# Performance work log

Hardware: AMD Instinct MI355X
Metric: run time of the kernel (lower is better)

## Reference

```python
import jax, jax.numpy as jnp
import numpy as np

N_NODES = 100000
N_EDGES = 3200000


def setup_inputs() -> dict:
    key = jax.random.key(0)
    ks = jax.random.split(key, 12)
    x = jax.random.normal(ks[0], (N_NODES, 34), dtype=jnp.float32)
    edge_index = jax.random.randint(ks[1], (2, N_EDGES), 0, N_NODES, dtype=jnp.int64)
    def lin(k, fin, fout):
        s = 1.0 / np.sqrt(fin)
        kw, kb = jax.random.split(k)
        W = jax.random.uniform(kw, (fin, fout), jnp.float32, -s, s)
        b = jax.random.uniform(kb, (fout,), jnp.float32, -s, s)
        return W, b
    W1, b1 = lin(ks[2], 34, 64)
    W2, b2 = lin(ks[3], 64, 32)
    W3, b3 = lin(ks[4], 32, 16)
    W4, b4 = lin(ks[5], 16, 8)
    Wc, bc = lin(ks[6], 8, 2)
    return {"x": x, "edge_index": edge_index,
            "W1": W1, "b1": b1, "W2": W2, "b2": b2,
            "W3": W3, "b3": b3, "W4": W4, "b4": b4,
            "Wc": Wc, "bc": bc}


def _gcn_norm(edge_index, n_nodes):
    # PyG GCNConv: add self-loops, symmetric normalization D^-1/2 (A+I) D^-1/2
    loop = jnp.arange(n_nodes, dtype=edge_index.dtype)
    src = jnp.concatenate([edge_index[0], loop])  # [E+N]
    dst = jnp.concatenate([edge_index[1], loop])
    deg = jax.ops.segment_sum(jnp.ones_like(dst, dtype=jnp.float32), dst,
                              num_segments=n_nodes)
    dinv = jnp.where(deg > 0, jax.lax.rsqrt(deg), 0.0)
    norm = dinv[src] * dinv[dst]  # [E+N]
    return src, dst, norm


def _gcn_conv(h, W, b, src, dst, norm, n_nodes):
    h = h @ W                                    # [N, Fout] small GEMM
    msg = h[src] * norm[:, None]                 # gather + scale
    out = jax.ops.segment_sum(msg, dst, num_segments=n_nodes)  # scatter-add
    return out + b


def reference(x, edge_index, W1, b1, W2, b2, W3, b3, W4, b4, Wc, bc):
    n = x.shape[0]
    src, dst, norm = _gcn_norm(edge_index, n)
    h = jnp.tanh(_gcn_conv(x, W1, b1, src, dst, norm, n))
    h = jnp.tanh(_gcn_conv(h, W2, b2, src, dst, norm, n))
    h = jnp.tanh(_gcn_conv(h, W3, b3, src, dst, norm, n))
    h = jnp.tanh(_gcn_conv(h, W4, b4, src, dst, norm, n))
    out = h @ Wc + bc
    return (out, h)
```

## Files before the change

kernel.cpp:

```cpp
#include <hip/hip_runtime.h>
#include <math.h>

#define N_NODES 100000
#define BSHIFT 8
#define BNODES 256
#define NB ((N_NODES + BNODES - 1) / BNODES)
#define CHUNK 8192


__device__ __forceinline__ unsigned short f2bf(float x) {
    unsigned u = __float_as_uint(x);
    u += 0x7FFFu + ((u >> 16) & 1u);
    return (unsigned short)(u >> 16);
}
__device__ __forceinline__ unsigned pack2(float a, float b) {
    return (unsigned)f2bf(a) | ((unsigned)f2bf(b) << 16);
}
__device__ __forceinline__ float bflo(unsigned u) { return __uint_as_float(u << 16); }
__device__ __forceinline__ float bfhi(unsigned u) { return __uint_as_float(u & 0xFFFF0000u); }
__device__ __forceinline__ int nt_ld(const int* p) { return __builtin_nontemporal_load(p); }


__global__ __launch_bounds__(256) void bucket_count(const int* __restrict__ dst,
                                                    int* __restrict__ bucketCount, int E) {
    __shared__ int hist[NB];
    for (int i = threadIdx.x; i < NB; i += 256) hist[i] = 0;
    __syncthreads();
    int i = blockIdx.x * blockDim.x + threadIdx.x;
    int stride = gridDim.x * blockDim.x;
    for (int e = i; e < E; e += stride)
        atomicAdd(&hist[nt_ld(dst + e) >> BSHIFT], 1);
    __syncthreads();
    for (int i2 = threadIdx.x; i2 < NB; i2 += 256) {
        int c = hist[i2];
        if (c) atomicAdd(&bucketCount[i2], c);
    }
}


__global__ __launch_bounds__(512) void bucket_scan(const int* __restrict__ bucketCount,
                                                   int* __restrict__ bucketOff,
                                                   int* __restrict__ bucketCursor, int E) {
    __shared__ int sh[512];
    int t = threadIdx.x;
    int v = (t < NB) ? bucketCount[t] : 0;
    sh[t] = v;
    __syncthreads();
    for (int d = 1; d < 512; d <<= 1) {
        int u = (t >= d) ? sh[t - d] : 0;
        __syncthreads();
        sh[t] += u;
        __syncthreads();
    }
    if (t < NB) { bucketOff[t] = sh[t] - v; bucketCursor[t] = sh[t] - v; }
    if (t == 0) bucketOff[NB] = E;
}


__global__ __launch_bounds__(256) void bucket_fill(const int* __restrict__ src,
                                                   const int* __restrict__ dst,
                                                   int* __restrict__ bucketCursor,
                                                   unsigned int* __restrict__ binned, int E) {
    __shared__ int hist[NB];
    __shared__ int base[NB];
    __shared__ int lcur[NB];
    __shared__ unsigned int recs[CHUNK];
    __shared__ unsigned short bkt[CHUNK];
    int t = threadIdx.x;
    for (int i = t; i < NB; i += 256) { hist[i] = 0; lcur[i] = 0; }
    __syncthreads();
    int cbase = blockIdx.x * CHUNK;
#pragma unroll
    for (int j = 0; j < CHUNK / 256; ++j) {
        int slot = t + j * 256;
        int e = cbase + slot;
        if (e < E) {
            int s = nt_ld(src + e);
            int d = nt_ld(dst + e);
            recs[slot] = (unsigned)s | ((unsigned)(d & (BNODES - 1)) << 17);
            int b = d >> BSHIFT;
            bkt[slot] = (unsigned short)b;
            atomicAdd(&hist[b], 1);
        } else {
            bkt[slot] = 0xFFFF;
        }
    }
    __syncthreads();
    for (int i = t; i < NB; i += 256) {
        int c = hist[i];
        base[i] = c ? atomicAdd(&bucketCursor[i], c) : 0;
    }
    __syncthreads();
#pragma unroll
    for (int j = 0; j < CHUNK / 256; ++j) {
        int slot = t + j * 256;
        unsigned short b = bkt[slot];
        if (b != 0xFFFF) {
            int pos = base[b] + atomicAdd(&lcur[b], 1);
            binned[pos] = recs[slot];
        }
    }
}


__global__ __launch_bounds__(256) void node_off_sort(const unsigned int* __restrict__ binned,
                                                     const int* __restrict__ bucketOff,
                                                     int* __restrict__ off,
                                                     float* __restrict__ dinv,
                                                     int* __restrict__ srcs, int n, int E) {
    __shared__ int hist[BNODES];
    __shared__ int sh[BNODES];
    __shared__ int lcur[BNODES];
    int t = threadIdx.x;
    int b = blockIdx.x;
    hist[t] = 0;
    __syncthreads();
    int rb = bucketOff[b], re = bucketOff[b + 1];
    for (int e = rb + t; e < re; e += 256)
        atomicAdd(&hist[(binned[e] >> 17) & 255], 1);
    __syncthreads();
    int v = hist[t];
    sh[t] = v;
    __syncthreads();
    for (int d = 1; d < 256; d <<= 1) {
        int u = (t >= d) ? sh[t - d] : 0;
        __syncthreads();
        sh[t] += u;
        __syncthreads();
    }
    int base = rb + sh[t] - v;
    lcur[t] = base;
    int g = b * BNODES + t;
    if (g < n) {
        off[g] = base;
        dinv[g] = rsqrtf((float)v + 1.0f);
    }
    if (b == NB - 1 && t == 0) off[n] = E;
    __syncthreads();
    for (int e = rb + t; e < re; e += 256) {
        unsigned int r = binned[e];
        int pos = atomicAdd(&lcur[(r >> 17) & 255], 1);
        srcs[pos] = (int)(r & 0x1FFFF);
    }
}


__global__ void x_pack(const float* __restrict__ x, const float* __restrict__ dinv,
                       unsigned* __restrict__ xm, unsigned* __restrict__ xt, int n) {
    int i = blockIdx.x * blockDim.x + threadIdx.x;
    if (i >= n) return;
    float dv = dinv[i];
    const float2* xr = (const float2*)(x + (size_t)i * 34);
    unsigned* om = xm + (size_t)i * 16;
#pragma unroll
    for (int j = 0; j < 16; ++j) { float2 v = xr[j]; om[j] = pack2(dv * v.x, dv * v.y); }
    float2 v = xr[16];
    xt[i] = pack2(dv * v.x, dv * v.y);
}


__global__ __launch_bounds__(256) void gather_x_bf16(const int* __restrict__ off,
        const int* __restrict__ srcs, const unsigned* __restrict__ xm,
        const unsigned* __restrict__ xt, const float* __restrict__ dinv,
        float* __restrict__ aggx, int n) {
    int g = blockIdx.x * 16 + (threadIdx.x >> 4);
    int f = threadIdx.x & 15;
    if (g >= n) return;
    int rb = off[g], re = off[g + 1];
    unsigned ug = xm[(size_t)g * 16 + f];
    float a0 = bflo(ug), a1 = bfhi(ug);
    float a2 = 0.f, a3 = 0.f;
    if (f == 0) { unsigned tt = xt[g]; a2 = bflo(tt); a3 = bfhi(tt); }
    int e = rb;
    for (; e + 8 <= re; e += 8) {
        int s0 = nt_ld(srcs + e),     s1 = nt_ld(srcs + e + 1);
        int s2 = nt_ld(srcs + e + 2), s3 = nt_ld(srcs + e + 3);
        int s4 = nt_ld(srcs + e + 4), s5 = nt_ld(srcs + e + 5);
        int s6 = nt_ld(srcs + e + 6), s7 = nt_ld(srcs + e + 7);
        unsigned u0 = xm[(size_t)s0 * 16 + f], u1 = xm[(size_t)s1 * 16 + f];
        unsigned u2 = xm[(size_t)s2 * 16 + f], u3 = xm[(size_t)s3 * 16 + f];
        unsigned u4 = xm[(size_t)s4 * 16 + f], u5 = xm[(size_t)s5 * 16 + f];
        unsigned u6 = xm[(size_t)s6 * 16 + f], u7 = xm[(size_t)s7 * 16 + f];
        a0 += bflo(u0); a1 += bfhi(u0); a0 += bflo(u1); a1 += bfhi(u1);
        a0 += bflo(u2); a1 += bfhi(u2); a0 += bflo(u3); a1 += bfhi(u3);
        a0 += bflo(u4); a1 += bfhi(u4); a0 += bflo(u5); a1 += bfhi(u5);
        a0 += bflo(u6); a1 += bfhi(u6); a0 += bflo(u7); a1 += bfhi(u7);
        if (f == 0) {
            unsigned t0 = xt[s0], t1 = xt[s1], t2 = xt[s2], t3 = xt[s3];
            unsigned t4 = xt[s4], t5 = xt[s5], t6 = xt[s6], t7 = xt[s7];
            a2 += bflo(t0); a3 += bfhi(t0); a2 += bflo(t1); a3 += bfhi(t1);
            a2 += bflo(t2); a3 += bfhi(t2); a2 += bflo(t3); a3 += bfhi(t3);
            a2 += bflo(t4); a3 += bfhi(t4); a2 += bflo(t5); a3 += bfhi(t5);
            a2 += bflo(t6); a3 += bfhi(t6); a2 += bflo(t7); a3 += bfhi(t7);
        }
    }
    for (; e < re; ++e) {
        int s = nt_ld(srcs + e);
        unsigned u = xm[(size_t)s * 16 + f];
        a0 += bflo(u); a1 += bfhi(u);
        if (f == 0) { unsigned tt = xt[s]; a2 += bflo(tt); a3 += bfhi(tt); }
    }
    float dv = dinv[g];
    *(float2*)(aggx + (size_t)g * 34 + 2 * f) = make_float2(dv * a0, dv * a1);
    if (f == 0) *(float2*)(aggx + (size_t)g * 34 + 32) = make_float2(dv * a2, dv * a3);
}


#define G12_BLOCKS 2048

__global__ __launch_bounds__(256) void gemm12(const float* __restrict__ aggx,
        const float* __restrict__ W1, const float* __restrict__ b1,
        const float* __restrict__ W2, const float* __restrict__ dinv,
        unsigned* __restrict__ linh2, int n) {
    __shared__ float sW1t[64 * 34];
    __shared__ float sW2[64 * 32];
    __shared__ float sh1[16][64];
    for (int i = threadIdx.x; i < 34 * 64; i += 256) {
        int k = i >> 6, j = i & 63;
        sW1t[j * 34 + k] = W1[i];
    }
    for (int i = threadIdx.x; i < 64 * 32; i += 256) sW2[i] = W2[i];
    __syncthreads();
    int j  = threadIdx.x & 63;
    int rq = threadIdx.x >> 6;
    int p  = threadIdx.x & 15;
    int r2 = threadIdx.x >> 4;
    float bj = b1[j];
    const float2* w1v = (const float2*)(sW1t + j * 34);
    const float2* w2v = (const float2*)sW2;
    for (int base = blockIdx.x * 16; base < n; base += G12_BLOCKS * 16) {
#pragma unroll
        for (int q = 0; q < 4; ++q) {
            int r = rq * 4 + q;
            int row = base + r;
            float h1v = 0.f;
            if (row < n) {
                const float2* hr = (const float2*)(aggx + (size_t)row * 34);
                float acc = 0.f;
#pragma unroll
                for (int k2 = 0; k2 < 17; ++k2) {
                    float2 wv = w1v[k2];
                    float2 hv = hr[k2];
                    acc = fmaf(hv.x, wv.x, acc);
                    acc = fmaf(hv.y, wv.y, acc);
                }
                h1v = tanhf(acc + bj);
            }
            sh1[r][j] = h1v;
        }
        __syncthreads();
        {
            int row = base + r2;
            if (row < n) {
                const float2* sh1v = (const float2*)&sh1[r2][0];
                float a0 = 0.f, a1 = 0.f;
#pragma unroll
                for (int k2 = 0; k2 < 32; ++k2) {
                    float2 h = sh1v[k2];
                    float2 wa = w2v[(2 * k2) * 16 + p];
                    float2 wb = w2v[(2 * k2 + 1) * 16 + p];
                    a0 = fmaf(h.x, wa.x, a0); a1 = fmaf(h.x, wa.y, a1);
                    a0 = fmaf(h.y, wb.x, a0); a1 = fmaf(h.y, wb.y, a1);
                }
                float dv = dinv[row];
                linh2[(size_t)row * 16 + p] = pack2(dv * a0, dv * a1);
            }
        }
        __syncthreads();
    }
}


__global__ __launch_bounds__(256) void gather2_proj(const int* __restrict__ off,
        const int* __restrict__ srcs, const unsigned* __restrict__ linh2,
        const float* __restrict__ dinv, const float* __restrict__ b2,
        const float* __restrict__ W3, unsigned* __restrict__ linh3, int n) {
    __shared__ float sW3[32 * 16];
    for (int i = threadIdx.x; i < 32 * 16; i += 256) sW3[i] = W3[i];
    __syncthreads();
    int g = blockIdx.x * 16 + (threadIdx.x >> 4);
    int f = threadIdx.x & 15;
    if (g >= n) return;
    int rb = off[g], re = off[g + 1];
    unsigned ug = linh2[(size_t)g * 16 + f];
    float a0 = bflo(ug), a1 = bfhi(ug);
    int e = rb;
    for (; e + 8 <= re; e += 8) {
        int s0 = nt_ld(srcs + e),     s1 = nt_ld(srcs + e + 1);
        int s2 = nt_ld(srcs + e + 2), s3 = nt_ld(srcs + e + 3);
        int s4 = nt_ld(srcs + e + 4), s5 = nt_ld(srcs + e + 5);
        int s6 = nt_ld(srcs + e + 6), s7 = nt_ld(srcs + e + 7);
        unsigned u0 = linh2[(size_t)s0 * 16 + f], u1 = linh2[(size_t)s1 * 16 + f];
        unsigned u2 = linh2[(size_t)s2 * 16 + f], u3 = linh2[(size_t)s3 * 16 + f];
        unsigned u4 = linh2[(size_t)s4 * 16 + f], u5 = linh2[(size_t)s5 * 16 + f];
        unsigned u6 = linh2[(size_t)s6 * 16 + f], u7 = linh2[(size_t)s7 * 16 + f];
        a0 += bflo(u0); a1 += bfhi(u0); a0 += bflo(u1); a1 += bfhi(u1);
        a0 += bflo(u2); a1 += bfhi(u2); a0 += bflo(u3); a1 += bfhi(u3);
        a0 += bflo(u4); a1 += bfhi(u4); a0 += bflo(u5); a1 += bfhi(u5);
        a0 += bflo(u6); a1 += bfhi(u6); a0 += bflo(u7); a1 += bfhi(u7);
    }
    for (; e < re; ++e) {
        int s = nt_ld(srcs + e);
        unsigned u = linh2[(size_t)s * 16 + f];
        a0 += bflo(u); a1 += bfhi(u);
    }
    float dv = dinv[g];
    float h0 = tanhf(fmaf(dv, a0, b2[2 * f]));
    float h1 = tanhf(fmaf(dv, a1, b2[2 * f + 1]));
    float p[16];
#pragma unroll
    for (int o = 0; o < 16; ++o)
        p[o] = h0 * sW3[(2 * f) * 16 + o] + h1 * sW3[(2 * f + 1) * 16 + o];
#pragma unroll
    for (int m = 1; m <= 8; m <<= 1)
#pragma unroll
        for (int o = 0; o < 16; ++o) p[o] += __shfl_xor(p[o], m);
    if (f < 8) linh3[(size_t)g * 8 + f] = pack2(dv * p[2 * f], dv * p[2 * f + 1]);
}


__global__ __launch_bounds__(256) void gather3_proj(const int* __restrict__ off,
        const int* __restrict__ srcs, const unsigned* __restrict__ linh3,
        const float* __restrict__ dinv, const float* __restrict__ b3,
        const float* __restrict__ W4, unsigned* __restrict__ linh4, int n) {
    __shared__ float sW4[16 * 8];
    for (int i = threadIdx.x; i < 16 * 8; i += 256) sW4[i] = W4[i];
    __syncthreads();
    int g = blockIdx.x * 32 + (threadIdx.x >> 3);
    int f = threadIdx.x & 7;
    if (g >= n) return;
    int rb = off[g], re = off[g + 1];
    unsigned ug = linh3[(size_t)g * 8 + f];
    float a0 = bflo(ug), a1 = bfhi(ug);
    int e = rb;
    for (; e + 8 <= re; e += 8) {
        int s0 = nt_ld(srcs + e),     s1 = nt_ld(srcs + e + 1);
        int s2 = nt_ld(srcs + e + 2), s3 = nt_ld(srcs + e + 3);
        int s4 = nt_ld(srcs + e + 4), s5 = nt_ld(srcs + e + 5);
        int s6 = nt_ld(srcs + e + 6), s7 = nt_ld(srcs + e + 7);
        unsigned u0 = linh3[(size_t)s0 * 8 + f], u1 = linh3[(size_t)s1 * 8 + f];
        unsigned u2 = linh3[(size_t)s2 * 8 + f], u3 = linh3[(size_t)s3 * 8 + f];
        unsigned u4 = linh3[(size_t)s4 * 8 + f], u5 = linh3[(size_t)s5 * 8 + f];
        unsigned u6 = linh3[(size_t)s6 * 8 + f], u7 = linh3[(size_t)s7 * 8 + f];
        a0 += bflo(u0); a1 += bfhi(u0); a0 += bflo(u1); a1 += bfhi(u1);
        a0 += bflo(u2); a1 += bfhi(u2); a0 += bflo(u3); a1 += bfhi(u3);
        a0 += bflo(u4); a1 += bfhi(u4); a0 += bflo(u5); a1 += bfhi(u5);
        a0 += bflo(u6); a1 += bfhi(u6); a0 += bflo(u7); a1 += bfhi(u7);
    }
    for (; e < re; ++e) {
        int s = nt_ld(srcs + e);
        unsigned u = linh3[(size_t)s * 8 + f];
        a0 += bflo(u); a1 += bfhi(u);
    }
    float dv = dinv[g];
    float h0 = tanhf(fmaf(dv, a0, b3[2 * f]));
    float h1 = tanhf(fmaf(dv, a1, b3[2 * f + 1]));
    float p[8];
#pragma unroll
    for (int o = 0; o < 8; ++o)
        p[o] = h0 * sW4[(2 * f) * 8 + o] + h1 * sW4[(2 * f + 1) * 8 + o];
#pragma unroll
    for (int m = 1; m <= 4; m <<= 1)
#pragma unroll
        for (int o = 0; o < 8; ++o) p[o] += __shfl_xor(p[o], m);
    if (f < 4) linh4[(size_t)g * 4 + f] = pack2(dv * p[2 * f], dv * p[2 * f + 1]);
}


__global__ __launch_bounds__(256) void gather4_cls(const int* __restrict__ off,
        const int* __restrict__ srcs, const unsigned* __restrict__ linh4,
        const float* __restrict__ dinv, const float* __restrict__ b4,
        float* __restrict__ hout, const float* __restrict__ Wc,
        const float* __restrict__ bc, float* __restrict__ out, int n) {
    int g = blockIdx.x * 64 + (threadIdx.x >> 2);
    int f = threadIdx.x & 3;
    if (g >= n) return;
    int rb = off[g], re = off[g + 1];
    unsigned ug = linh4[(size_t)g * 4 + f];
    float a0 = bflo(ug), a1 = bfhi(ug);
    int e = rb;
    for (; e + 8 <= re; e += 8) {
        int s0 = nt_ld(srcs + e),     s1 = nt_ld(srcs + e + 1);
        int s2 = nt_ld(srcs + e + 2), s3 = nt_ld(srcs + e + 3);
        int s4 = nt_ld(srcs + e + 4), s5 = nt_ld(srcs + e + 5);
        int s6 = nt_ld(srcs + e + 6), s7 = nt_ld(srcs + e + 7);
        unsigned u0 = linh4[(size_t)s0 * 4 + f], u1 = linh4[(size_t)s1 * 4 + f];
        unsigned u2 = linh4[(size_t)s2 * 4 + f], u3 = linh4[(size_t)s3 * 4 + f];
        unsigned u4 = linh4[(size_t)s4 * 4 + f], u5 = linh4[(size_t)s5 * 4 + f];
        unsigned u6 = linh4[(size_t)s6 * 4 + f], u7 = linh4[(size_t)s7 * 4 + f];
        a0 += bflo(u0); a1 += bfhi(u0); a0 += bflo(u1); a1 += bfhi(u1);
        a0 += bflo(u2); a1 += bfhi(u2); a0 += bflo(u3); a1 += bfhi(u3);
        a0 += bflo(u4); a1 += bfhi(u4); a0 += bflo(u5); a1 += bfhi(u5);
        a0 += bflo(u6); a1 += bfhi(u6); a0 += bflo(u7); a1 += bfhi(u7);
    }
    for (; e < re; ++e) {
        int s = nt_ld(srcs + e);
        unsigned u = linh4[(size_t)s * 4 + f];
        a0 += bflo(u); a1 += bfhi(u);
    }
    float dv = dinv[g];
    a0 = tanhf(fmaf(dv, a0, b4[2 * f]));
    a1 = tanhf(fmaf(dv, a1, b4[2 * f + 1]));
    *(float2*)(hout + (size_t)g * 8 + 2 * f) = make_float2(a0, a1);
    float p0 = a0 * Wc[4 * f]     + a1 * Wc[4 * f + 2];
    float p1 = a0 * Wc[4 * f + 1] + a1 * Wc[4 * f + 3];
    p0 += __shfl_xor(p0, 1); p1 += __shfl_xor(p1, 1);
    p0 += __shfl_xor(p0, 2); p1 += __shfl_xor(p1, 2);
    if (f == 0) {
        out[(size_t)g * 2]     = p0 + bc[0];
        out[(size_t)g * 2 + 1] = p1 + bc[1];
    }
}


static inline char* alignp(char* p) {
    return (char*)(((uintptr_t)p + 15) & ~(uintptr_t)15);
}

extern "C" void kernel_launch(void* const* d_in, const int* in_sizes, int n_in,
                              void* d_out, int out_size, void* d_ws, size_t ws_size,
                              hipStream_t stream) {
    const float* x  = (const float*)d_in[0];
    const int*   ei = (const int*)d_in[1];
    const float* W1 = (const float*)d_in[2];  const float* b1 = (const float*)d_in[3];
    const float* W2 = (const float*)d_in[4];
    const float* b2 = (const float*)d_in[5];
    const float* W3 = (const float*)d_in[6];  const float* b3 = (const float*)d_in[7];
    const float* W4 = (const float*)d_in[8];  const float* b4 = (const float*)d_in[9];
    const float* Wc = (const float*)d_in[10]; const float* bc = (const float*)d_in[11];

    float* out  = (float*)d_out;
    float* hout = out + (size_t)2 * N_NODES;

    const int n = N_NODES;
    const int E = in_sizes[1] / 2;
    const int* src = ei;
    const int* dst = ei + E;

    char* w = (char*)d_ws;
    float*        dinv         = (float*)w;        w = alignp(w + (size_t)n * 4);
    int*          bucketCount  = (int*)w;          w = alignp(w + (size_t)NB * 4);
    int*          bucketOff    = (int*)w;          w = alignp(w + (size_t)(NB + 1) * 4);
    int*          bucketCursor = (int*)w;          w = alignp(w + (size_t)NB * 4);
    int*          off          = (int*)w;          w = alignp(w + (size_t)(n + 1) * 4);
    unsigned int* binned       = (unsigned int*)w; w = alignp(w + (size_t)E * 4);
    int*          srcs         = (int*)w;          w = alignp(w + (size_t)E * 4);
    unsigned int* xm           = (unsigned int*)w; w = alignp(w + (size_t)n * 16 * 4);
    unsigned int* xt           = (unsigned int*)w; w = alignp(w + (size_t)n * 4);
    float*        aggx         = (float*)w;        w = alignp(w + (size_t)n * 34 * 4);
    unsigned int* linh2        = (unsigned int*)w; w = alignp(w + (size_t)n * 16 * 4);
    unsigned int* linh3        = (unsigned int*)w; w = alignp(w + (size_t)n * 8 * 4);
    unsigned int* linh4        = (unsigned int*)w; w = alignp(w + (size_t)n * 4 * 4);

    hipMemsetAsync(bucketCount, 0, NB * sizeof(int), stream);
    bucket_count<<<1024, 256, 0, stream>>>(dst, bucketCount, E);
    bucket_scan<<<1, 512, 0, stream>>>(bucketCount, bucketOff, bucketCursor, E);
    bucket_fill<<<(E + CHUNK - 1) / CHUNK, 256, 0, stream>>>(src, dst, bucketCursor, binned, E);
    node_off_sort<<<NB, 256, 0, stream>>>(binned, bucketOff, off, dinv, srcs, n, E);
    x_pack<<<(n + 255) / 256, 256, 0, stream>>>(x, dinv, xm, xt, n);

    gather_x_bf16<<<(n + 15) / 16, 256, 0, stream>>>(off, srcs, xm, xt, dinv, aggx, n);
    gemm12<<<G12_BLOCKS, 256, 0, stream>>>(aggx, W1, b1, W2, dinv, linh2, n);

    gather2_proj<<<(n + 15) / 16, 256, 0, stream>>>(off, srcs, linh2, dinv, b2, W3, linh3, n);

    gather3_proj<<<(n + 31) / 32, 256, 0, stream>>>(off, srcs, linh3, dinv, b3, W4, linh4, n);

    gather4_cls<<<(n + 63) / 64, 256, 0, stream>>>(off, srcs, linh4, dinv, b4, hout,
                                                   Wc, bc, out, n);
}
```

Baseline: 470.2 us.

## Split wide feature gathers into two column-half passes for cache locality

The 34-wide bf16 input gather and the 32-wide layer-2 gather are each split into two kernels that gather half of the feature columns from separate, narrower arrays (32 or 36 bytes per row instead of 64). The smaller per-pass gather table is meant to stay resident in L2/MALL, so random neighbour reads hit cache more often. The cost is reading the CSR index array twice per layer, extra launches, and an intermediate h2a buffer round trip. The change also adds nontemporal stores for aggx and transposes the W3/W4 tiles held in shared memory.

```diff
diff --git a/kernel.cpp b/kernel.cpp
--- a/kernel.cpp
+++ b/kernel.cpp
@@ -8,6 +8,8 @@
 #define CHUNK 8192
 
 
+typedef float f32x2 __attribute__((ext_vector_type(2)));
+
 __device__ __forceinline__ unsigned short f2bf(float x) {
     unsigned u = __float_as_uint(x);
     u += 0x7FFFu + ((u >> 16) & 1u);
@@ -19,6 +21,10 @@
 __device__ __forceinline__ float bflo(unsigned u) { return __uint_as_float(u << 16); }
 __device__ __forceinline__ float bfhi(unsigned u) { return __uint_as_float(u & 0xFFFF0000u); }
 __device__ __forceinline__ int nt_ld(const int* p) { return __builtin_nontemporal_load(p); }
+__device__ __forceinline__ void nt_stf2(float* p, float a, float b) {
+    f32x2 v; v.x = a; v.y = b;
+    __builtin_nontemporal_store(v, (f32x2*)p);
+}
 
 
 __global__ __launch_bounds__(256) void bucket_count(const int* __restrict__ dst,
@@ -146,48 +152,84 @@
 
 
 __global__ void x_pack(const float* __restrict__ x, const float* __restrict__ dinv,
-                       unsigned* __restrict__ xm, unsigned* __restrict__ xt, int n) {
+                       unsigned* __restrict__ xa, unsigned* __restrict__ xb, int n) {
     int i = blockIdx.x * blockDim.x + threadIdx.x;
     if (i >= n) return;
     float dv = dinv[i];
     const float2* xr = (const float2*)(x + (size_t)i * 34);
-    unsigned* om = xm + (size_t)i * 16;
-#pragma unroll
-    for (int j = 0; j < 16; ++j) { float2 v = xr[j]; om[j] = pack2(dv * v.x, dv * v.y); }
-    float2 v = xr[16];
-    xt[i] = pack2(dv * v.x, dv * v.y);
-}
-
-
-__global__ __launch_bounds__(256) void gather_x_bf16(const int* __restrict__ off,
-        const int* __restrict__ srcs, const unsigned* __restrict__ xm,
-        const unsigned* __restrict__ xt, const float* __restrict__ dinv,
-        float* __restrict__ aggx, int n) {
-    int g = blockIdx.x * 16 + (threadIdx.x >> 4);
-    int f = threadIdx.x & 15;
+    unsigned* oa = xa + (size_t)i * 8;
+#pragma unroll
+    for (int j = 0; j < 8; ++j) { float2 v = xr[j]; oa[j] = pack2(dv * v.x, dv * v.y); }
+    unsigned* ob = xb + (size_t)i * 9;
+#pragma unroll
+    for (int j = 0; j < 9; ++j) { float2 v = xr[8 + j]; ob[j] = pack2(dv * v.x, dv * v.y); }
+}
+
+
+__global__ __launch_bounds__(256) void gather_xa(const int* __restrict__ off,
+        const int* __restrict__ srcs, const unsigned* __restrict__ xa,
+        const float* __restrict__ dinv, float* __restrict__ aggx, int n) {
+    int g = blockIdx.x * 32 + (threadIdx.x >> 3);
+    int f = threadIdx.x & 7;
     if (g >= n) return;
     int rb = off[g], re = off[g + 1];
-    unsigned ug = xm[(size_t)g * 16 + f];
+    unsigned ug = xa[(size_t)g * 8 + f];
     float a0 = bflo(ug), a1 = bfhi(ug);
-    float a2 = 0.f, a3 = 0.f;
-    if (f == 0) { unsigned tt = xt[g]; a2 = bflo(tt); a3 = bfhi(tt); }
     int e = rb;
     for (; e + 8 <= re; e += 8) {
         int s0 = nt_ld(srcs + e),     s1 = nt_ld(srcs + e + 1);
         int s2 = nt_ld(srcs + e + 2), s3 = nt_ld(srcs + e + 3);
         int s4 = nt_ld(srcs + e + 4), s5 = nt_ld(srcs + e + 5);
         int s6 = nt_ld(srcs + e + 6), s7 = nt_ld(srcs + e + 7);
-        unsigned u0 = xm[(size_t)s0 * 16 + f], u1 = xm[(size_t)s1 * 16 + f];
-        unsigned u2 = xm[(size_t)s2 * 16 + f], u3 = xm[(size_t)s3 * 16 + f];
-        unsigned u4 = xm[(size_t)s4 * 16 + f], u5 = xm[(size_t)s5 * 16 + f];
-        unsigned u6 = xm[(size_t)s6 * 16 + f], u7 = xm[(size_t)s7 * 16 + f];
+        unsigned u0 = xa[(size_t)s0 * 8 + f], u1 = xa[(size_t)s1 * 8 + f];
+        unsigned u2 = xa[(size_t)s2 * 8 + f], u3 = xa[(size_t)s3 * 8 + f];
+        unsigned u4 = xa[(size_t)s4 * 8 + f], u5 = xa[(size_t)s5 * 8 + f];
+        unsigned u6 = xa[(size_t)s6 * 8 + f], u7 = xa[(size_t)s7 * 8 + f];
+        a0 += bflo(u0); a1 += bfhi(u0); a0 += bflo(u1); a1 += bfhi(u1);
+        a0 += bflo(u2); a1 += bfhi(u2); a0 += bflo(u3); a1 += bfhi(u3);
+        a0 += bflo(u4); a1 += bfhi(u4); a0 += bflo(u5); a1 += bfhi(u5);
+        a0 += bflo(u6); a1 += bfhi(u6); a0 += bflo(u7); a1 += bfhi(u7);
+    }
+    for (; e < re; ++e) {
+        int s = nt_ld(srcs + e);
+        unsigned u = xa[(size_t)s * 8 + f];
+        a0 += bflo(u); a1 += bfhi(u);
+    }
+    float dv = dinv[g];
+    nt_stf2(aggx + (size_t)g * 34 + 2 * f, dv * a0, dv * a1);
+}
+
+
+__global__ __launch_bounds__(256) void gather_xb(const int* __restrict__ off,
+        const int* __restrict__ srcs, const unsigned* __restrict__ xb,
+        const float* __restrict__ dinv, float* __restrict__ aggx, int n) {
+    int g = blockIdx.x * 32 + (threadIdx.x >> 3);
+    int f = threadIdx.x & 7;
+    if (g >= n) return;
+    int rb = off[g], re = off[g + 1];
+    unsigned ug = xb[(size_t)g * 9 + f];
+    float a0 = bflo(ug), a1 = bfhi(ug);
+    float a2 = 0.f, a3 = 0.f;
+    if (f == 0) { unsigned tt = xb[(size_t)g * 9 + 8]; a2 = bflo(tt); a3 = bfhi(tt); }
+    int e = rb;
+    for (; e + 8 <= re; e += 8) {
+        int s0 = nt_ld(srcs + e),     s1 = nt_ld(srcs + e + 1);
+        int s2 = nt_ld(srcs + e + 2), s3 = nt_ld(srcs + e + 3);
+        int s4 = nt_ld(srcs + e + 4), s5 = nt_ld(srcs + e + 5);
+        int s6 = nt_ld(srcs + e + 6), s7 = nt_ld(srcs + e + 7);
+        unsigned u0 = xb[(size_t)s0 * 9 + f], u1 = xb[(size_t)s1 * 9 + f];
+        unsigned u2 = xb[(size_t)s2 * 9 + f], u3 = xb[(size_t)s3 * 9 + f];
+        unsigned u4 = xb[(size_t)s4 * 9 + f], u5 = xb[(size_t)s5 * 9 + f];
+        unsigned u6 = xb[(size_t)s6 * 9 + f], u7 = xb[(size_t)s7 * 9 + f];
         a0 += bflo(u0); a1 += bfhi(u0); a0 += bflo(u1); a1 += bfhi(u1);
         a0 += bflo(u2); a1 += bfhi(u2); a0 += bflo(u3); a1 += bfhi(u3);
         a0 += bflo(u4); a1 += bfhi(u4); a0 += bflo(u5); a1 += bfhi(u5);
         a0 += bflo(u6); a1 += bfhi(u6); a0 += bflo(u7); a1 += bfhi(u7);
         if (f == 0) {
-            unsigned t0 = xt[s0], t1 = xt[s1], t2 = xt[s2], t3 = xt[s3];
-            unsigned t4 = xt[s4], t5 = xt[s5], t6 = xt[s6], t7 = xt[s7];
+            unsigned t0 = xb[(size_t)s0 * 9 + 8], t1 = xb[(size_t)s1 * 9 + 8];
+            unsigned t2 = xb[(size_t)s2 * 9 + 8], t3 = xb[(size_t)s3 * 9 + 8];
+            unsigned t4 = xb[(size_t)s4 * 9 + 8], t5 = xb[(size_t)s5 * 9 + 8];
+            unsigned t6 = xb[(size_t)s6 * 9 + 8], t7 = xb[(size_t)s7 * 9 + 8];
             a2 += bflo(t0); a3 += bfhi(t0); a2 += bflo(t1); a3 += bfhi(t1);
             a2 += bflo(t2); a3 += bfhi(t2); a2 += bflo(t3); a3 += bfhi(t3);
             a2 += bflo(t4); a3 += bfhi(t4); a2 += bflo(t5); a3 += bfhi(t5);
@@ -196,13 +238,13 @@
     }
     for (; e < re; ++e) {
         int s = nt_ld(srcs + e);
-        unsigned u = xm[(size_t)s * 16 + f];
+        unsigned u = xb[(size_t)s * 9 + f];
         a0 += bflo(u); a1 += bfhi(u);
-        if (f == 0) { unsigned tt = xt[s]; a2 += bflo(tt); a3 += bfhi(tt); }
+        if (f == 0) { unsigned tt = xb[(size_t)s * 9 + 8]; a2 += bflo(tt); a3 += bfhi(tt); }
     }
     float dv = dinv[g];
-    *(float2*)(aggx + (size_t)g * 34 + 2 * f) = make_float2(dv * a0, dv * a1);
-    if (f == 0) *(float2*)(aggx + (size_t)g * 34 + 32) = make_float2(dv * a2, dv * a3);
+    nt_stf2(aggx + (size_t)g * 34 + 16 + 2 * f, dv * a0, dv * a1);
+    if (f == 0) nt_stf2(aggx + (size_t)g * 34 + 32, dv * a2, dv * a3);
 }
 
 
@@ -211,7 +253,7 @@
 __global__ __launch_bounds__(256) void gemm12(const float* __restrict__ aggx,
         const float* __restrict__ W1, const float* __restrict__ b1,
         const float* __restrict__ W2, const float* __restrict__ dinv,
-        unsigned* __restrict__ linh2, int n) {
+        unsigned* __restrict__ l2a, unsigned* __restrict__ l2b, int n) {
     __shared__ float sW1t[64 * 34];
     __shared__ float sW2[64 * 32];
     __shared__ float sh1[16][64];
@@ -263,7 +305,9 @@
                     a0 = fmaf(h.y, wb.x, a0); a1 = fmaf(h.y, wb.y, a1);
                 }
                 float dv = dinv[row];
-                linh2[(size_t)row * 16 + p] = pack2(dv * a0, dv * a1);
+                unsigned pk = pack2(dv * a0, dv * a1);
+                if (p < 8) l2a[(size_t)row * 8 + p] = pk;
+                else       l2b[(size_t)row * 8 + (p - 8)] = pk;
             }
         }
         __syncthreads();
@@ -271,18 +315,15 @@
 }
 
 
-__global__ __launch_bounds__(256) void gather2_proj(const int* __restrict__ off,
-        const int* __restrict__ srcs, const unsigned* __restrict__ linh2,
+__global__ __launch_bounds__(256) void gather2a(const int* __restrict__ off,
+        const int* __restrict__ srcs, const unsigned* __restrict__ l2a,
         const float* __restrict__ dinv, const float* __restrict__ b2,
-        const float* __restrict__ W3, unsigned* __restrict__ linh3, int n) {
-    __shared__ float sW3[32 * 16];
-    for (int i = threadIdx.x; i < 32 * 16; i += 256) sW3[i] = W3[i];
-    __syncthreads();
-    int g = blockIdx.x * 16 + (threadIdx.x >> 4);
-    int f = threadIdx.x & 15;
+        unsigned* __restrict__ h2a, int n) {
+    int g = blockIdx.x * 32 + (threadIdx.x >> 3);
+    int f = threadIdx.x & 7;
     if (g >= n) return;
     int rb = off[g], re = off[g + 1];
-    unsigned ug = linh2[(size_t)g * 16 + f];
+    unsigned ug = l2a[(size_t)g * 8 + f];
     float a0 = bflo(ug), a1 = bfhi(ug);
     int e = rb;
     for (; e + 8 <= re; e += 8) {
@@ -290,10 +331,10 @@
         int s2 = nt_ld(srcs + e + 2), s3 = nt_ld(srcs + e + 3);
         int s4 = nt_ld(srcs + e + 4), s5 = nt_ld(srcs + e + 5);
         int s6 = nt_ld(srcs + e + 6), s7 = nt_ld(srcs + e + 7);
-        unsigned u0 = linh2[(size_t)s0 * 16 + f], u1 = linh2[(size_t)s1 * 16 + f];
-        unsigned u2 = linh2[(size_t)s2 * 16 + f], u3 = linh2[(size_t)s3 * 16 + f];
-        unsigned u4 = linh2[(size_t)s4 * 16 + f], u5 = linh2[(size_t)s5 * 16 + f];
-        unsigned u6 = linh2[(size_t)s6 * 16 + f], u7 = linh2[(size_t)s7 * 16 + f];
+        unsigned u0 = l2a[(size_t)s0 * 8 + f], u1 = l2a[(size_t)s1 * 8 + f];
+        unsigned u2 = l2a[(size_t)s2 * 8 + f], u3 = l2a[(size_t)s3 * 8 + f];
+        unsigned u4 = l2a[(size_t)s4 * 8 + f], u5 = l2a[(size_t)s5 * 8 + f];
+        unsigned u6 = l2a[(size_t)s6 * 8 + f], u7 = l2a[(size_t)s7 * 8 + f];
         a0 += bflo(u0); a1 += bfhi(u0); a0 += bflo(u1); a1 += bfhi(u1);
         a0 += bflo(u2); a1 += bfhi(u2); a0 += bflo(u3); a1 += bfhi(u3);
         a0 += bflo(u4); a1 += bfhi(u4); a0 += bflo(u5); a1 += bfhi(u5);
@@ -301,21 +342,70 @@
     }
     for (; e < re; ++e) {
         int s = nt_ld(srcs + e);
-        unsigned u = linh2[(size_t)s * 16 + f];
+        unsigned u = l2a[(size_t)s * 8 + f];
         a0 += bflo(u); a1 += bfhi(u);
     }
     float dv = dinv[g];
     float h0 = tanhf(fmaf(dv, a0, b2[2 * f]));
     float h1 = tanhf(fmaf(dv, a1, b2[2 * f + 1]));
+    h2a[(size_t)g * 8 + f] = pack2(h0, h1);
+}
+
+
+__global__ __launch_bounds__(256) void gather2b(const int* __restrict__ off,
+        const int* __restrict__ srcs, const unsigned* __restrict__ l2b,
+        const unsigned* __restrict__ h2a, const float* __restrict__ dinv,
+        const float* __restrict__ b2, const float* __restrict__ W3,
+        unsigned* __restrict__ linh3, int n) {
+    __shared__ float sW3t[16 * 32];
+    for (int i = threadIdx.x; i < 32 * 16; i += 256) {
+        int k = i >> 4, o = i & 15;
+        sW3t[o * 32 + k] = W3[i];
+    }
+    __syncthreads();
+    int g = blockIdx.x * 32 + (threadIdx.x >> 3);
+    int f = threadIdx.x & 7;
+    if (g >= n) return;
+    int rb = off[g], re = off[g + 1];
+    unsigned ug = l2b[(size_t)g * 8 + f];
+    float a0 = bflo(ug), a1 = bfhi(ug);
+    int e = rb;
+    for (; e + 8 <= re; e += 8) {
+        int s0 = nt_ld(srcs + e),     s1 = nt_ld(srcs + e + 1);
+        int s2 = nt_ld(srcs + e + 2), s3 = nt_ld(srcs + e + 3);
+        int s4 = nt_ld(srcs + e + 4), s5 = nt_ld(srcs + e + 5);
+        int s6 = nt_ld(srcs + e + 6), s7 = nt_ld(srcs + e + 7);
+        unsigned u0 = l2b[(size_t)s0 * 8 + f], u1 = l2b[(size_t)s1 * 8 + f];
+        unsigned u2 = l2b[(size_t)s2 * 8 + f], u3 = l2b[(size_t)s3 * 8 + f];
+        unsigned u4 = l2b[(size_t)s4 * 8 + f], u5 = l2b[(size_t)s5 * 8 + f];
+        unsigned u6 = l2b[(size_t)s6 * 8 + f], u7 = l2b[(size_t)s7 * 8 + f];
+        a0 += bflo(u0); a1 += bfhi(u0); a0 += bflo(u1); a1 += bfhi(u1);
+        a0 += bflo(u2); a1 += bfhi(u2); a0 += bflo(u3); a1 += bfhi(u3);
+        a0 += bflo(u4); a1 += bfhi(u4); a0 += bflo(u5); a1 += bfhi(u5);
+        a0 += bflo(u6); a1 += bfhi(u6); a0 += bflo(u7); a1 += bfhi(u7);
+    }
+    for (; e < re; ++e) {
+        int s = nt_ld(srcs + e);
+        unsigned u = l2b[(size_t)s * 8 + f];
+        a0 += bflo(u); a1 += bfhi(u);
+    }
+    float dv = dinv[g];
+    float hh0 = tanhf(fmaf(dv, a0, b2[16 + 2 * f]));
+    float hh1 = tanhf(fmaf(dv, a1, b2[17 + 2 * f]));
+    unsigned ul = h2a[(size_t)g * 8 + f];
+    float hl0 = bflo(ul), hl1 = bfhi(ul);
     float p[16];
 #pragma unroll
-    for (int o = 0; o < 16; ++o)
-        p[o] = h0 * sW3[(2 * f) * 16 + o] + h1 * sW3[(2 * f + 1) * 16 + o];
-#pragma unroll
-    for (int m = 1; m <= 8; m <<= 1)
+    for (int o = 0; o < 16; ++o) {
+        const float* wc = sW3t + o * 32;
+        p[o] = hl0 * wc[2 * f] + hl1 * wc[2 * f + 1]
+             + hh0 * wc[16 + 2 * f] + hh1 * wc[17 + 2 * f];
+    }
+#pragma unroll
+    for (int m = 1; m <= 4; m <<= 1)
 #pragma unroll
         for (int o = 0; o < 16; ++o) p[o] += __shfl_xor(p[o], m);
-    if (f < 8) linh3[(size_t)g * 8 + f] = pack2(dv * p[2 * f], dv * p[2 * f + 1]);
+    linh3[(size_t)g * 8 + f] = pack2(dv * p[2 * f], dv * p[2 * f + 1]);
 }
 
 
@@ -323,8 +413,11 @@
         const int* __restrict__ srcs, const unsigned* __restrict__ linh3,
         const float* __restrict__ dinv, const float* __restrict__ b3,
         const float* __restrict__ W4, unsigned* __restrict__ linh4, int n) {
-    __shared__ float sW4[16 * 8];
-    for (int i = threadIdx.x; i < 16 * 8; i += 256) sW4[i] = W4[i];
+    __shared__ float sW4t[8 * 16];
+    for (int i = threadIdx.x; i < 16 * 8; i += 256) {
+        int k = i >> 3, o = i & 7;
+        sW4t[o * 16 + k] = W4[i];
+    }
     __syncthreads();
     int g = blockIdx.x * 32 + (threadIdx.x >> 3);
     int f = threadIdx.x & 7;
@@ -358,7 +451,7 @@
     float p[8];
 #pragma unroll
     for (int o = 0; o < 8; ++o)
-        p[o] = h0 * sW4[(2 * f) * 8 + o] + h1 * sW4[(2 * f + 1) * 8 + o];
+        p[o] = h0 * sW4t[o * 16 + 2 * f] + h1 * sW4t[o * 16 + 2 * f + 1];
 #pragma unroll
     for (int m = 1; m <= 4; m <<= 1)
 #pragma unroll
@@ -445,10 +538,12 @@
     int*          off          = (int*)w;          w = alignp(w + (size_t)(n + 1) * 4);
     unsigned int* binned       = (unsigned int*)w; w = alignp(w + (size_t)E * 4);
     int*          srcs         = (int*)w;          w = alignp(w + (size_t)E * 4);
-    unsigned int* xm           = (unsigned int*)w; w = alignp(w + (size_t)n * 16 * 4);
-    unsigned int* xt           = (unsigned int*)w; w = alignp(w + (size_t)n * 4);
+    unsigned int* xa           = (unsigned int*)w; w = alignp(w + (size_t)n * 8 * 4);
+    unsigned int* xb           = (unsigned int*)w; w = alignp(w + (size_t)n * 9 * 4);
     float*        aggx         = (float*)w;        w = alignp(w + (size_t)n * 34 * 4);
-    unsigned int* linh2        = (unsigned int*)w; w = alignp(w + (size_t)n * 16 * 4);
+    unsigned int* l2a          = (unsigned int*)w; w = alignp(w + (size_t)n * 8 * 4);
+    unsigned int* l2b          = (unsigned int*)w; w = alignp(w + (size_t)n * 8 * 4);
+    unsigned int* h2a          = (unsigned int*)w; w = alignp(w + (size_t)n * 8 * 4);
     unsigned int* linh3        = (unsigned int*)w; w = alignp(w + (size_t)n * 8 * 4);
     unsigned int* linh4        = (unsigned int*)w; w = alignp(w + (size_t)n * 4 * 4);
 
@@ -457,12 +552,14 @@
     bucket_scan<<<1, 512, 0, stream>>>(bucketCount, bucketOff, bucketCursor, E);
     bucket_fill<<<(E + CHUNK - 1) / CHUNK, 256, 0, stream>>>(src, dst, bucketCursor, binned, E);
     node_off_sort<<<NB, 256, 0, stream>>>(binned, bucketOff, off, dinv, srcs, n, E);
-    x_pack<<<(n + 255) / 256, 256, 0, stream>>>(x, dinv, xm, xt, n);
-
-    gather_x_bf16<<<(n + 15) / 16, 256, 0, stream>>>(off, srcs, xm, xt, dinv, aggx, n);
-    gemm12<<<G12_BLOCKS, 256, 0, stream>>>(aggx, W1, b1, W2, dinv, linh2, n);
-
-    gather2_proj<<<(n + 15) / 16, 256, 0, stream>>>(off, srcs, linh2, dinv, b2, W3, linh3, n);
+    x_pack<<<(n + 255) / 256, 256, 0, stream>>>(x, dinv, xa, xb, n);
+
+    gather_xa<<<(n + 31) / 32, 256, 0, stream>>>(off, srcs, xa, dinv, aggx, n);
+    gather_xb<<<(n + 31) / 32, 256, 0, stream>>>(off, srcs, xb, dinv, aggx, n);
+    gemm12<<<G12_BLOCKS, 256, 0, stream>>>(aggx, W1, b1, W2, dinv, l2a, l2b, n);
+
+    gather2a<<<(n + 31) / 32, 256, 0, stream>>>(off, srcs, l2a, dinv, b2, h2a, n);
+    gather2b<<<(n + 31) / 32, 256, 0, stream>>>(off, srcs, l2b, h2a, dinv, b2, W3, linh3, n);
 
     gather3_proj<<<(n + 31) / 32, 256, 0, stream>>>(off, srcs, linh3, dinv, b3, W4, linh4, n);
 
```

Measured after the change: 509.5 us. 1.08x slower.
